# Kernel optimization log

Measured on AMD Instinct MI355X. Metric: run time of the kernel, lower is better.

Reference implementation:

```python
import jax, jax.numpy as jnp
import numpy as np

B, I, R, A, V = 256, 512, 512, 196, 10000

def _linear_params(key, out_dim, in_dim):
    k1, k2 = jax.random.split(key)
    s = 1.0 / np.sqrt(in_dim)
    W = jax.random.uniform(k1, (out_dim, in_dim), minval=-s, maxval=s, dtype=jnp.float32)
    b = jax.random.uniform(k2, (out_dim,), minval=-s, maxval=s, dtype=jnp.float32)
    return W, b

def setup_inputs() -> dict:
    key = jax.random.key(0)
    ks = jax.random.split(key, 16)
    d = {}
    d['x'] = jax.random.normal(ks[0], (B, I), dtype=jnp.float32)
    d['att'] = jax.random.normal(ks[1], (B, A, R), dtype=jnp.float32)
    d['prev_c'] = jax.random.normal(ks[2], (B, R), dtype=jnp.float32)
    d['prev_h'] = jax.random.normal(ks[3], (B, R), dtype=jnp.float32)
    for i, (name, o, inn) in enumerate([('a2a', A, R), ('h2a', A, R), ('d2d', 1, A),
                                         ('i2h', 4 * R, I), ('a2h', 4 * R, R), ('h2h', 4 * R, R),
                                         ('a2a1', A, R), ('h2a1', A, R), ('d2d1', 1, A),
                                         ('proj', V, R)]):
        W, b = _linear_params(ks[4 + i], o, inn)
        d['W_' + name] = W
        d['b_' + name] = b
    return d

def _lin(x, W, b):
    return x @ W.T + b

def _attend(att, h, Wa, ba, Wh, bh, Wd, bd):
    # att: (B, A, R); h: (B, R)
    av = jnp.einsum('bar,or->bao', att, Wa) + ba        # (B, A, A)
    ah = _lin(h, Wh, bh)                                # (B, A)
    dot = jnp.tanh(av + ah[:, :, None])                 # (B, A, A)
    scores = jnp.einsum('bao,o->ba', dot, Wd[0]) + bd[0]  # (B, A)
    w = jax.nn.softmax(scores, axis=-1)
    return jnp.einsum('bar,ba->br', att, w)             # (B, R)

def reference(x, att, prev_c, prev_h,
              W_a2a, b_a2a, W_h2a, b_h2a, W_d2d, b_d2d,
              W_i2h, b_i2h, W_a2h, b_a2h, W_h2h, b_h2h,
              W_a2a1, b_a2a1, W_h2a1, b_h2a1, W_d2d1, b_d2d1,
              W_proj, b_proj):
    # first attention uses prev_h
    prev_att_res = _attend(att, prev_h, W_a2a, b_a2a, W_h2a, b_h2a, W_d2d, b_d2d)
    sums = _lin(x, W_i2h, b_i2h) + _lin(prev_h, W_h2h, b_h2h) + _lin(prev_att_res, W_a2h, b_a2h)
    sig = jax.nn.sigmoid(sums[:, :3 * R])
    in_gate = sig[:, 0:R]
    forget_gate = sig[:, R:2 * R]
    out_gate = sig[:, 2 * R:3 * R]
    in_transform = jnp.tanh(sums[:, 3 * R:4 * R])
    next_c = forget_gate * prev_c + in_gate * in_transform
    next_h = out_gate * jnp.tanh(next_c)
    # second attention uses next_h
    att_res = _attend(att, next_h, W_a2a1, b_a2a1, W_h2a1, b_h2a1, W_d2d1, b_d2d1)
    top_h = att_res + next_h
    logsoft = jax.nn.log_softmax(_lin(top_h, W_proj, b_proj), axis=-1)
    return next_c, top_h, logsoft
```

## Files before the change

kernel.cpp:

```cpp
#include <hip/hip_runtime.h>
#include <math.h>

constexpr int cB  = 256;
constexpr int cI  = 512;
constexpr int cR  = 512;
constexpr int cA  = 196;
constexpr int cV  = 10000;
constexpr int cH4 = 2048;

typedef short bf16x8 __attribute__((ext_vector_type(8)));
typedef float f32x4  __attribute__((ext_vector_type(4)));
typedef unsigned short us8 __attribute__((ext_vector_type(8)));

__device__ inline unsigned short f2bf(float f) {
    unsigned int u = __float_as_uint(f);
    u += 0x7fffu + ((u >> 16) & 1u);
    return (unsigned short)(u >> 16);
}
__device__ inline float bf2f(unsigned short s) {
    return __uint_as_float(((unsigned int)s) << 16);
}
__device__ inline float tanh_f(float x) {
    return 1.f - 2.f / (1.f + __expf(2.f * x));
}

__global__ __launch_bounds__(256) void k_cvt_ah(
    const float* __restrict__ s0, unsigned short* __restrict__ d0, int nb0,
    const float* __restrict__ s1, unsigned short* __restrict__ d1, int nb1,
    const float* __restrict__ s2, unsigned short* __restrict__ d2, int nb2,
    const float* __restrict__ s3, unsigned short* __restrict__ d3, int nb3,
    const float* __restrict__ h, const float* __restrict__ W,
    const float* __restrict__ bias, float* __restrict__ outah)
{
    __shared__ __align__(16) float h_s[cR];
    int blk = blockIdx.x;
    int ncvt = nb0 + nb1 + nb2 + nb3;
    int t = threadIdx.x;
    if (blk < ncvt) {
        const float* src; unsigned short* dst; int base;
        if (blk < nb0)                  { src = s0; dst = d0; base = blk; }
        else if (blk < nb0 + nb1)       { src = s1; dst = d1; base = blk - nb0; }
        else if (blk < nb0 + nb1 + nb2) { src = s2; dst = d2; base = blk - nb0 - nb1; }
        else                            { src = s3; dst = d3; base = blk - nb0 - nb1 - nb2; }
        int i = base * 256 + t;
        float4 v = ((const float4*)src)[i];
        ushort4 b;
        b.x = f2bf(v.x); b.y = f2bf(v.y); b.z = f2bf(v.z); b.w = f2bf(v.w);
        ((ushort4*)dst)[i] = b;
    } else {
        int b = blk - ncvt;
        h_s[t]       = h[b * cR + t];
        h_s[t + 256] = h[b * cR + t + 256];
        __syncthreads();
        if (t < cA) {
            const float4* Wv = (const float4*)(W + (size_t)t * cR);
            const float4* hv = (const float4*)h_s;
            float acc = 0.f;
            #pragma unroll 4
            for (int k = 0; k < cR / 4; ++k) {
                float4 w4 = Wv[k], x4 = hv[k];
                acc += w4.x * x4.x + w4.y * x4.y + w4.z * x4.z + w4.w * x4.w;
            }
            outah[b * cA + t] = acc + bias[t];
        }
    }
}

__global__ __launch_bounds__(256) void k_ah(
    const float* __restrict__ h, const float* __restrict__ W,
    const float* __restrict__ bias, float* __restrict__ out)
{
    __shared__ __align__(16) float h_s[cR];
    int b = blockIdx.x;
    int t = threadIdx.x;
    h_s[t]       = h[b * cR + t];
    h_s[t + 256] = h[b * cR + t + 256];
    __syncthreads();
    if (t < cA) {
        const float4* Wv = (const float4*)(W + (size_t)t * cR);
        const float4* hv = (const float4*)h_s;
        float acc = 0.f;
        #pragma unroll 4
        for (int k = 0; k < cR / 4; ++k) {
            float4 w4 = Wv[k], x4 = hv[k];
            acc += w4.x * x4.x + w4.y * x4.y + w4.z * x4.z + w4.w * x4.w;
        }
        out[b * cA + t] = acc + bias[t];
    }
}

constexpr int SC_LDA = 72;

__global__ __launch_bounds__(256, 2) void k_scores_cv(
    const float* __restrict__ att, unsigned short* __restrict__ att_bf,
    const unsigned short* __restrict__ wa_bf,
    const float* __restrict__ ba, const float* __restrict__ Wd,
    const float* __restrict__ bd, const float* __restrict__ ah,
    float* __restrict__ scores, int wb)
{
    __shared__ __align__(16) unsigned short att_s[128][SC_LDA];
    __shared__ __align__(16) unsigned short wa_s[224][SC_LDA];
    __shared__ float ba_s[224];
    __shared__ float wd_s[224];
    __shared__ float part_s[128][2];

    int tid  = threadIdx.x;
    int wave = tid >> 6;
    int lane = tid & 63;
    int lx   = lane & 15;
    int quad = lane >> 4;
    int mg   = wave >> 1;
    int ng   = wave & 1;
    size_t row0 = (size_t)blockIdx.x * 128;

    if (tid < 224) {
        ba_s[tid] = (tid < cA) ? ba[tid] : 0.f;
        wd_s[tid] = (tid < cA) ? Wd[tid] : 0.f;
    }

    int a_r = tid >> 4, a_c = (tid & 15) * 4;
    int w_r = tid >> 3, w_c = (tid & 7) * 8;
    const float* attA = att + (row0 + a_r) * cR + a_c;
    unsigned short* wbA = att_bf + (row0 + a_r) * cR + a_c;

    f32x4 acc[4][7];
    #pragma unroll
    for (int m = 0; m < 4; ++m)
        #pragma unroll
        for (int c = 0; c < 7; ++c) acc[m][c] = (f32x4){0.f, 0.f, 0.f, 0.f};

    float4 patt[8];
    us8    pwa[7];
    #pragma unroll
    for (int i = 0; i < 8; ++i)
        patt[i] = *(const float4*)(attA + (size_t)i * 16 * cR);
    #pragma unroll
    for (int i = 0; i < 7; ++i) {
        int r = w_r + 32 * i;
        pwa[i] = (r < cA) ? *(const us8*)(wa_bf + (size_t)r * cR + w_c)
                          : (us8){0,0,0,0,0,0,0,0};
    }

    for (int k0 = 0; k0 < cR; k0 += 64) {
        #pragma unroll
        for (int i = 0; i < 8; ++i) {
            float4 v = patt[i];
            ushort4 bv;
            bv.x = f2bf(v.x); bv.y = f2bf(v.y); bv.z = f2bf(v.z); bv.w = f2bf(v.w);
            *(ushort4*)&att_s[a_r + 16 * i][a_c] = bv;
            if (wb)
                *(ushort4*)(wbA + (size_t)i * 16 * cR + k0) = bv;
        }
        #pragma unroll
        for (int i = 0; i < 7; ++i)
            *(us8*)&wa_s[w_r + 32 * i][w_c] = pwa[i];
        if (k0 + 64 < cR) {
            #pragma unroll
            for (int i = 0; i < 8; ++i)
                patt[i] = *(const float4*)(attA + (size_t)i * 16 * cR + k0 + 64);
            #pragma unroll
            for (int i = 0; i < 7; ++i) {
                int r = w_r + 32 * i;
                pwa[i] = (r < cA) ? *(const us8*)(wa_bf + (size_t)r * cR + k0 + 64 + w_c)
                                  : (us8){0,0,0,0,0,0,0,0};
            }
        }
        __syncthreads();
        #pragma unroll
        for (int ks = 0; ks < 2; ++ks) {
            int kb = ks * 32 + quad * 8;
            bf16x8 af[4];
            #pragma unroll
            for (int m = 0; m < 4; ++m)
                af[m] = *(const bf16x8*)&att_s[mg * 64 + m * 16 + lx][kb];
            #pragma unroll
            for (int c = 0; c < 7; ++c) {
                bf16x8 bfr = *(const bf16x8*)&wa_s[ng * 112 + c * 16 + lx][kb];
                #pragma unroll
                for (int m = 0; m < 4; ++m)
                    acc[m][c] = __builtin_amdgcn_mfma_f32_16x16x32_bf16(af[m], bfr, acc[m][c], 0, 0, 0);
            }
        }
        __syncthreads();
    }

    #pragma unroll
    for (int m = 0; m < 4; ++m) {
        #pragma unroll
        for (int reg = 0; reg < 4; ++reg) {
            int rl = mg * 64 + m * 16 + quad * 4 + reg;
            float ahv = ah[row0 + rl];
            float part = 0.f;
            #pragma unroll
            for (int c = 0; c < 7; ++c) {
                int col = ng * 112 + c * 16 + lx;
                part += tanh_f(acc[m][c][reg] + ba_s[col] + ahv) * wd_s[col];
            }
            part += __shfl_xor(part, 1);
            part += __shfl_xor(part, 2);
            part += __shfl_xor(part, 4);
            part += __shfl_xor(part, 8);
            if (lx == 0) part_s[rl][ng] = part;
        }
    }
    __syncthreads();
    if (tid < 128)
        scores[row0 + tid] = part_s[tid][0] + part_s[tid][1] + bd[0];
}

__global__ __launch_bounds__(256, 2) void k_scores_bf(
    const unsigned short* __restrict__ att_bf,
    const unsigned short* __restrict__ wa_bf,
    const float* __restrict__ ba, const float* __restrict__ Wd,
    const float* __restrict__ bd, const float* __restrict__ ah,
    float* __restrict__ scores)
{
    __shared__ __align__(16) unsigned short att_s[128][SC_LDA];
    __shared__ __align__(16) unsigned short wa_s[224][SC_LDA];
    __shared__ float ba_s[224];
    __shared__ float wd_s[224];
    __shared__ float part_s[128][2];

    int tid  = threadIdx.x;
    int wave = tid >> 6;
    int lane = tid & 63;
    int lx   = lane & 15;
    int quad = lane >> 4;
    int mg   = wave >> 1;
    int ng   = wave & 1;
    size_t row0 = (size_t)blockIdx.x * 128;

    if (tid < 224) {
        ba_s[tid] = (tid < cA) ? ba[tid] : 0.f;
        wd_s[tid] = (tid < cA) ? Wd[tid] : 0.f;
    }

    int a_r = tid >> 3, a_c = (tid & 7) * 8;
    int w_r = tid >> 3, w_c = (tid & 7) * 8;
    const unsigned short* attA = att_bf + (row0 + a_r) * cR + a_c;

    f32x4 acc[4][7];
    #pragma unroll
    for (int m = 0; m < 4; ++m)
        #pragma unroll
        for (int c = 0; c < 7; ++c) acc[m][c] = (f32x4){0.f, 0.f, 0.f, 0.f};

    us8 patt[4];
    us8 pwa[7];
    #pragma unroll
    for (int i = 0; i < 4; ++i)
        patt[i] = *(const us8*)(attA + (size_t)i * 32 * cR);
    #pragma unroll
    for (int i = 0; i < 7; ++i) {
        int r = w_r + 32 * i;
        pwa[i] = (r < cA) ? *(const us8*)(wa_bf + (size_t)r * cR + w_c)
                          : (us8){0,0,0,0,0,0,0,0};
    }

    for (int k0 = 0; k0 < cR; k0 += 64) {
        #pragma unroll
        for (int i = 0; i < 4; ++i)
            *(us8*)&att_s[a_r + 32 * i][a_c] = patt[i];
        #pragma unroll
        for (int i = 0; i < 7; ++i)
            *(us8*)&wa_s[w_r + 32 * i][w_c] = pwa[i];
        if (k0 + 64 < cR) {
            #pragma unroll
            for (int i = 0; i < 4; ++i)
                patt[i] = *(const us8*)(attA + (size_t)i * 32 * cR + k0 + 64);
            #pragma unroll
            for (int i = 0; i < 7; ++i) {
                int r = w_r + 32 * i;
                pwa[i] = (r < cA) ? *(const us8*)(wa_bf + (size_t)r * cR + k0 + 64 + w_c)
                                  : (us8){0,0,0,0,0,0,0,0};
            }
        }
        __syncthreads();
        #pragma unroll
        for (int ks = 0; ks < 2; ++ks) {
            int kb = ks * 32 + quad * 8;
            bf16x8 af[4];
            #pragma unroll
            for (int m = 0; m < 4; ++m)
                af[m] = *(const bf16x8*)&att_s[mg * 64 + m * 16 + lx][kb];
            #pragma unroll
            for (int c = 0; c < 7; ++c) {
                bf16x8 bfr = *(const bf16x8*)&wa_s[ng * 112 + c * 16 + lx][kb];
                #pragma unroll
                for (int m = 0; m < 4; ++m)
                    acc[m][c] = __builtin_amdgcn_mfma_f32_16x16x32_bf16(af[m], bfr, acc[m][c], 0, 0, 0);
            }
        }
        __syncthreads();
    }

    #pragma unroll
    for (int m = 0; m < 4; ++m) {
        #pragma unroll
        for (int reg = 0; reg < 4; ++reg) {
            int rl = mg * 64 + m * 16 + quad * 4 + reg;
            float ahv = ah[row0 + rl];
            float part = 0.f;
            #pragma unroll
            for (int c = 0; c < 7; ++c) {
                int col = ng * 112 + c * 16 + lx;
                part += tanh_f(acc[m][c][reg] + ba_s[col] + ahv) * wd_s[col];
            }
            part += __shfl_xor(part, 1);
            part += __shfl_xor(part, 2);
            part += __shfl_xor(part, 4);
            part += __shfl_xor(part, 8);
            if (lx == 0) part_s[rl][ng] = part;
        }
    }
    __syncthreads();
    if (tid < 128)
        scores[row0 + tid] = part_s[tid][0] + part_s[tid][1] + bd[0];
}

__device__ inline void softmax_w(const float* scores, int b, int t, float* red,
                                 float* w_s)
{
    float s = (t < cA) ? scores[b * cA + t] : -INFINITY;
    red[t] = s; __syncthreads();
    for (int off = 128; off > 0; off >>= 1) {
        if (t < off) red[t] = fmaxf(red[t], red[t + off]);
        __syncthreads();
    }
    float mx = red[0];
    __syncthreads();
    float e = (t < cA) ? __expf(s - mx) : 0.f;
    red[t] = e; __syncthreads();
    for (int off = 128; off > 0; off >>= 1) {
        if (t < off) red[t] += red[t + off];
        __syncthreads();
    }
    float inv = 1.f / red[0];
    if (t < cA) w_s[t] = e * inv;
    __syncthreads();
}

__global__ __launch_bounds__(256) void k_attres_bf(
    const float* __restrict__ scores, const unsigned short* __restrict__ att_bf,
    const float* __restrict__ addin,
    float* __restrict__ out, unsigned short* __restrict__ out_bf)
{
    __shared__ float red[256];
    __shared__ float w_s[cA];
    __shared__ float red2[4][512];
    int b = blockIdx.x, t = threadIdx.x;
    softmax_w(scores, b, t, red, w_s);

    int p = t >> 6, l = t & 63;
    const unsigned short* base = att_bf + (size_t)b * cA * cR + l * 8;
    float acc[8] = {};
    #pragma unroll 7
    for (int a = p; a < cA; a += 4) {
        us8 v = *(const us8*)(base + (size_t)a * cR);
        float w = w_s[a];
        #pragma unroll
        for (int j = 0; j < 8; ++j)
            acc[j] += bf2f(v[j]) * w;
    }
    #pragma unroll
    for (int j = 0; j < 8; ++j)
        red2[p][l * 8 + j] = acc[j];
    __syncthreads();
    #pragma unroll
    for (int rr = 0; rr < 2; ++rr) {
        int r = t + rr * 256;
        float s = red2[0][r] + red2[1][r] + red2[2][r] + red2[3][r];
        if (addin) s += addin[b * cR + r];
        out[b * cR + r] = s;
        out_bf[b * cR + r] = f2bf(s);
    }
}

__global__ __launch_bounds__(256) void k_attres_f32(
    const float* __restrict__ scores, const float* __restrict__ att,
    const float* __restrict__ addin,
    float* __restrict__ out, unsigned short* __restrict__ out_bf)
{
    __shared__ float red[256];
    __shared__ float w_s[cA];
    int b = blockIdx.x, t = threadIdx.x;
    softmax_w(scores, b, t, red, w_s);

    const float* attb = att + (size_t)b * cA * cR + 2 * t;
    float acc0 = 0.f, acc1 = 0.f;
    #pragma unroll 4
    for (int a = 0; a < cA; ++a) {
        float2 u = *(const float2*)(attb + (size_t)a * cR);
        float w = w_s[a];
        acc0 += u.x * w;
        acc1 += u.y * w;
    }
    if (addin) {
        acc0 += addin[b * cR + 2 * t];
        acc1 += addin[b * cR + 2 * t + 1];
    }
    out[b * cR + 2 * t]     = acc0;
    out[b * cR + 2 * t + 1] = acc1;
    out_bf[b * cR + 2 * t]     = f2bf(acc0);
    out_bf[b * cR + 2 * t + 1] = f2bf(acc1);
}

__global__ __launch_bounds__(256, 4) void k_sums(
    const unsigned short* __restrict__ x_bf,
    const unsigned short* __restrict__ h_bf,
    const unsigned short* __restrict__ ar_bf,
    const float* __restrict__ Wi, const float* __restrict__ Wh,
    const float* __restrict__ Wa,
    const float* __restrict__ bi, const float* __restrict__ bh,
    const float* __restrict__ ba, float* __restrict__ out)
{
    __shared__ __align__(16) unsigned short a_s[32][SC_LDA];
    __shared__ __align__(16) unsigned short w_s[64][SC_LDA];
    int tid  = threadIdx.x;
    int wave = tid >> 6;
    int lane = tid & 63;
    int lx   = lane & 15;
    int quad = lane >> 4;
    int b0 = blockIdx.x * 32;
    int j0 = blockIdx.y * 64;

    const unsigned short* Aarr[3] = {x_bf, h_bf, ar_bf};
    const float* Warr[3] = {Wi, Wh, Wa};

    int a_r = tid >> 3, a_c = (tid & 7) * 8;
    int w_r = tid >> 4, w_c = (tid & 15) * 4;

    f32x4 acc0 = {0.f, 0.f, 0.f, 0.f}, acc1 = {0.f, 0.f, 0.f, 0.f};

    us8 pa;
    float4 pw[4];
    pa = *(const us8*)(Aarr[0] + (size_t)(b0 + a_r) * cR + a_c);
    #pragma unroll
    for (int i = 0; i < 4; ++i)
        pw[i] = *(const float4*)(Warr[0] + (size_t)(j0 + w_r + 16 * i) * cR + w_c);

    for (int it = 0; it < 24; ++it) {
        *(us8*)&a_s[a_r][a_c] = pa;
        #pragma unroll
        for (int i = 0; i < 4; ++i) {
            float4 v = pw[i];
            ushort4 bv;
            bv.x = f2bf(v.x); bv.y = f2bf(v.y); bv.z = f2bf(v.z); bv.w = f2bf(v.w);
            *(ushort4*)&w_s[w_r + 16 * i][w_c] = bv;
        }
        if (it < 23) {
            int s2 = (it + 1) >> 3, k2 = ((it + 1) & 7) * 64;
            pa = *(const us8*)(Aarr[s2] + (size_t)(b0 + a_r) * cR + k2 + a_c);
            #pragma unroll
            for (int i = 0; i < 4; ++i)
                pw[i] = *(const float4*)(Warr[s2] + (size_t)(j0 + w_r + 16 * i) * cR + k2 + w_c);
        }
        __syncthreads();
        #pragma unroll
        for (int ks = 0; ks < 2; ++ks) {
            int kb = ks * 32 + quad * 8;
            bf16x8 afr0 = *(const bf16x8*)&a_s[lx][kb];
            bf16x8 afr1 = *(const bf16x8*)&a_s[16 + lx][kb];
            bf16x8 bfr  = *(const bf16x8*)&w_s[wave * 16 + lx][kb];
            acc0 = __builtin_amdgcn_mfma_f32_16x16x32_bf16(afr0, bfr, acc0, 0, 0, 0);
            acc1 = __builtin_amdgcn_mfma_f32_16x16x32_bf16(afr1, bfr, acc1, 0, 0, 0);
        }
        __syncthreads();
    }
    int j = j0 + wave * 16 + lx;
    float bsum = bi[j] + bh[j] + ba[j];
    #pragma unroll
    for (int reg = 0; reg < 4; ++reg) {
        int b = b0 + quad * 4 + reg;
        out[(size_t)b * cH4 + j]        = acc0[reg] + bsum;
        out[(size_t)(b + 16) * cH4 + j] = acc1[reg] + bsum;
    }
}

__global__ __launch_bounds__(256, 3) void k_lin(
    const unsigned short* __restrict__ in_bf, const float* __restrict__ W,
    const float* __restrict__ bias, float* __restrict__ out, int N)
{
    __shared__ __align__(16) unsigned short a_s[128][SC_LDA];
    __shared__ __align__(16) unsigned short w_s[64][SC_LDA];
    int tid  = threadIdx.x;
    int wave = tid >> 6;
    int lane = tid & 63;
    int lx   = lane & 15;
    int quad = lane >> 4;
    int mg   = wave >> 1;
    int ng   = wave & 1;
    int b0 = blockIdx.x * 128;
    int j0 = blockIdx.y * 64;

    int a_r = tid >> 3, a_c = (tid & 7) * 8;
    int w_r = tid >> 4, w_c = (tid & 15) * 4;

    f32x4 acc[4][2];
    #pragma unroll
    for (int m = 0; m < 4; ++m)
        #pragma unroll
        for (int c = 0; c < 2; ++c) acc[m][c] = (f32x4){0.f, 0.f, 0.f, 0.f};

    us8 pa[4];
    float4 pw[4];
    #pragma unroll
    for (int i = 0; i < 4; ++i)
        pa[i] = *(const us8*)(in_bf + (size_t)(b0 + a_r + 32 * i) * cR + a_c);
    #pragma unroll
    for (int i = 0; i < 4; ++i) {
        int r = j0 + w_r + 16 * i;
        pw[i] = (r < N) ? *(const float4*)(W + (size_t)r * cR + w_c)
                        : make_float4(0.f, 0.f, 0.f, 0.f);
    }

    for (int k0 = 0; k0 < cR; k0 += 64) {
        #pragma unroll
        for (int i = 0; i < 4; ++i)
            *(us8*)&a_s[a_r + 32 * i][a_c] = pa[i];
        #pragma unroll
        for (int i = 0; i < 4; ++i) {
            float4 v = pw[i];
            ushort4 bv;
            bv.x = f2bf(v.x); bv.y = f2bf(v.y); bv.z = f2bf(v.z); bv.w = f2bf(v.w);
            *(ushort4*)&w_s[w_r + 16 * i][w_c] = bv;
        }
        if (k0 + 64 < cR) {
            #pragma unroll
            for (int i = 0; i < 4; ++i)
                pa[i] = *(const us8*)(in_bf + (size_t)(b0 + a_r + 32 * i) * cR + k0 + 64 + a_c);
            #pragma unroll
            for (int i = 0; i < 4; ++i) {
                int r = j0 + w_r + 16 * i;
                pw[i] = (r < N) ? *(const float4*)(W + (size_t)r * cR + k0 + 64 + w_c)
                                : make_float4(0.f, 0.f, 0.f, 0.f);
            }
        }
        __syncthreads();
        #pragma unroll
        for (int ks = 0; ks < 2; ++ks) {
            int kb = ks * 32 + quad * 8;
            bf16x8 af[4];
            #pragma unroll
            for (int m = 0; m < 4; ++m)
                af[m] = *(const bf16x8*)&a_s[mg * 64 + m * 16 + lx][kb];
            #pragma unroll
            for (int c = 0; c < 2; ++c) {
                bf16x8 bfr = *(const bf16x8*)&w_s[ng * 32 + c * 16 + lx][kb];
                #pragma unroll
                for (int m = 0; m < 4; ++m)
                    acc[m][c] = __builtin_amdgcn_mfma_f32_16x16x32_bf16(af[m], bfr, acc[m][c], 0, 0, 0);
            }
        }
        __syncthreads();
    }
    #pragma unroll
    for (int c = 0; c < 2; ++c) {
        int j = j0 + ng * 32 + c * 16 + lx;
        if (j < N) {
            float bv = bias[j];
            #pragma unroll
            for (int m = 0; m < 4; ++m) {
                #pragma unroll
                for (int reg = 0; reg < 4; ++reg) {
                    int b = b0 + mg * 64 + m * 16 + quad * 4 + reg;
                    out[(size_t)b * N + j] = acc[m][c][reg] + bv;
                }
            }
        }
    }
}

__global__ __launch_bounds__(256) void k_cell(
    const float* __restrict__ sums, const float* __restrict__ prev_c,
    float* __restrict__ next_c, float* __restrict__ next_h)
{
    int idx = blockIdx.x * 256 + threadIdx.x;
    int b = idx >> 9;
    int j = idx & 511;
    const float* srow = sums + (size_t)b * cH4;
    float ig = 1.f / (1.f + __expf(-srow[j]));
    float fg = 1.f / (1.f + __expf(-srow[cR + j]));
    float og = 1.f / (1.f + __expf(-srow[2 * cR + j]));
    float gt = tanh_f(srow[3 * cR + j]);
    float c = fg * prev_c[idx] + ig * gt;
    float hh = og * tanh_f(c);
    next_c[idx] = c;
    next_h[idx] = hh;
}

__global__ __launch_bounds__(256) void k_logsoftmax(float* __restrict__ logits)
{
    __shared__ float red[256];
    int b = blockIdx.x, t = threadIdx.x;
    float* row = logits + (size_t)b * cV;
    const float4* row4 = (const float4*)row;
    float mx = -INFINITY;
    for (int v = t; v < cV / 4; v += 256) {
        float4 f = row4[v];
        mx = fmaxf(mx, fmaxf(fmaxf(f.x, f.y), fmaxf(f.z, f.w)));
    }
    red[t] = mx; __syncthreads();
    for (int off = 128; off > 0; off >>= 1) {
        if (t < off) red[t] = fmaxf(red[t], red[t + off]);
        __syncthreads();
    }
    mx = red[0]; __syncthreads();
    float sum = 0.f;
    for (int v = t; v < cV / 4; v += 256) {
        float4 f = row4[v];
        sum += __expf(f.x - mx) + __expf(f.y - mx) + __expf(f.z - mx) + __expf(f.w - mx);
    }
    red[t] = sum; __syncthreads();
    for (int off = 128; off > 0; off >>= 1) {
        if (t < off) red[t] += red[t + off];
        __syncthreads();
    }
    float lse = mx + logf(red[0]);
    for (int v = t; v < cV / 4; v += 256) {
        float4 f = row4[v];
        f.x -= lse; f.y -= lse; f.z -= lse; f.w -= lse;
        ((float4*)row)[v] = f;
    }
}

extern "C" void kernel_launch(void* const* d_in, const int* in_sizes, int n_in,
                              void* d_out, int out_size, void* d_ws, size_t ws_size,
                              hipStream_t stream)
{
    const float* x      = (const float*)d_in[0];
    const float* att    = (const float*)d_in[1];
    const float* prev_c = (const float*)d_in[2];
    const float* prev_h = (const float*)d_in[3];
    const float* W_a2a  = (const float*)d_in[4];
    const float* b_a2a  = (const float*)d_in[5];
    const float* W_h2a  = (const float*)d_in[6];
    const float* b_h2a  = (const float*)d_in[7];
    const float* W_d2d  = (const float*)d_in[8];
    const float* b_d2d  = (const float*)d_in[9];
    const float* W_i2h  = (const float*)d_in[10];
    const float* b_i2h  = (const float*)d_in[11];
    const float* W_a2h  = (const float*)d_in[12];
    const float* b_a2h  = (const float*)d_in[13];
    const float* W_h2h  = (const float*)d_in[14];
    const float* b_h2h  = (const float*)d_in[15];
    const float* W_a2a1 = (const float*)d_in[16];
    const float* b_a2a1 = (const float*)d_in[17];
    const float* W_h2a1 = (const float*)d_in[18];
    const float* b_h2a1 = (const float*)d_in[19];
    const float* W_d2d1 = (const float*)d_in[20];
    const float* b_d2d1 = (const float*)d_in[21];
    const float* W_proj = (const float*)d_in[22];
    const float* b_proj = (const float*)d_in[23];

    float* out_next_c = (float*)d_out;
    float* out_top_h  = out_next_c + (size_t)cB * cR;
    float* out_logits = out_top_h  + (size_t)cB * cR;

    const size_t ATT_FLOATS = 12845056;
    const size_t NEED_A = (ATT_FLOATS + 1445888) * sizeof(float);
    bool bigws = ws_size >= NEED_A;

    float* ws = (float*)d_ws;
    unsigned short* att_bf = (unsigned short*)ws;
    float* p = bigws ? (ws + ATT_FLOATS) : ws;
    unsigned short* wa2a_bf  = (unsigned short*)p;  p += 50176;
    unsigned short* wa2a1_bf = (unsigned short*)p;  p += 50176;
    unsigned short* x_bf     = (unsigned short*)p;  p += 65536;
    unsigned short* h_bf     = (unsigned short*)p;  p += 65536;
    unsigned short* ar1_bf   = (unsigned short*)p;  p += 65536;
    unsigned short* ar2_bf   = (unsigned short*)p;  p += 65536;
    unsigned short* toph_bf  = (unsigned short*)p;  p += 65536;
    float* ws_ah      = p;  p += 50176;
    float* ws_scores  = p;  p += 50176;
    float* ws_attres1 = p;  p += 131072;
    float* ws_attres2 = p;  p += 131072;
    float* ws_sums    = p;  p += 524288;
    float* ws_next_h  = p;  p += 131072;

    k_cvt_ah<<<452 + cB, 256, 0, stream>>>(W_a2a, wa2a_bf, 98,
                                           W_a2a1, wa2a1_bf, 98,
                                           x, x_bf, 128,
                                           prev_h, h_bf, 128,
                                           prev_h, W_h2a, b_h2a, ws_ah);

    k_scores_cv<<<(cB * cA) / 128, 256, 0, stream>>>(att, att_bf, wa2a_bf,
                                                     b_a2a, W_d2d, b_d2d,
                                                     ws_ah, ws_scores,
                                                     bigws ? 1 : 0);
    if (bigws)
        k_attres_bf<<<cB, 256, 0, stream>>>(ws_scores, att_bf, nullptr,
                                            ws_attres1, ar1_bf);
    else
        k_attres_f32<<<cB, 256, 0, stream>>>(ws_scores, att, nullptr,
                                             ws_attres1, ar1_bf);

    k_sums<<<dim3(8, 32), 256, 0, stream>>>(x_bf, h_bf, ar1_bf,
                                            W_i2h, W_h2h, W_a2h,
                                            b_i2h, b_h2h, b_a2h, ws_sums);
    k_cell<<<(cB * cR) / 256, 256, 0, stream>>>(ws_sums, prev_c, out_next_c, ws_next_h);

    k_ah<<<cB, 256, 0, stream>>>(ws_next_h, W_h2a1, b_h2a1, ws_ah);
    if (bigws) {
        k_scores_bf<<<(cB * cA) / 128, 256, 0, stream>>>(att_bf, wa2a1_bf,
                                                         b_a2a1, W_d2d1, b_d2d1,
                                                         ws_ah, ws_scores);
        k_attres_bf<<<cB, 256, 0, stream>>>(ws_scores, att_bf, ws_next_h,
                                            out_top_h, toph_bf);
    } else {
        k_scores_cv<<<(cB * cA) / 128, 256, 0, stream>>>(att, att_bf, wa2a1_bf,
                                                         b_a2a1, W_d2d1, b_d2d1,
                                                         ws_ah, ws_scores, 0);
        k_attres_f32<<<cB, 256, 0, stream>>>(ws_scores, att, ws_next_h,
                                             out_top_h, toph_bf);
    }

    k_lin<<<dim3(2, 157), 256, 0, stream>>>(toph_bf, W_proj, b_proj, out_logits, cV);
    k_logsoftmax<<<cB, 256, 0, stream>>>(out_logits);
}
```

Measured before the change: 362.4 us.

## Compute both attention projections in one MFMA pass and fuse cell with h2a

A new scores kernel multiplies each att tile against both W_a2a and W_a2a1 in one pass. It finishes the first attention's scores and stores the second attention's pre-activation projection (bf16) to workspace, so the second large GEMM becomes a light tanh-dot kernel once next_h is known. The LSTM cell is fused with the h2a linear, attres uses 512 threads, and logsoftmax uses a single-pass online max/sum. This needs about 20 MB of extra workspace and falls back to the old path when the workspace is too small.

```diff
diff --git a/kernel.cpp b/kernel.cpp
--- a/kernel.cpp
+++ b/kernel.cpp
@@ -7,6 +7,7 @@
 constexpr int cA  = 196;
 constexpr int cV  = 10000;
 constexpr int cH4 = 2048;
+constexpr int AV2_LD = 200;
 
 typedef short bf16x8 __attribute__((ext_vector_type(8)));
 typedef float f32x4  __attribute__((ext_vector_type(4)));
@@ -91,6 +92,181 @@
 
 constexpr int SC_LDA = 72;
 
+__global__ __launch_bounds__(512, 2) void k_scores2g(
+    const float* __restrict__ att, unsigned short* __restrict__ att_bf,
+    const unsigned short* __restrict__ wa1_bf,
+    const unsigned short* __restrict__ wa2_bf,
+    const float* __restrict__ ba1, const float* __restrict__ ba2,
+    const float* __restrict__ Wd1, const float* __restrict__ bd1,
+    const float* __restrict__ ah, float* __restrict__ scores,
+    unsigned short* __restrict__ av2)
+{
+    __shared__ __align__(16) unsigned short att_s[128][SC_LDA];
+    __shared__ __align__(16) unsigned short wa_s[448][SC_LDA];
+    __shared__ float ba1_s[224];
+    __shared__ float ba2_s[224];
+    __shared__ float wd_s[224];
+    __shared__ float part_s[128][2];
+
+    int tid  = threadIdx.x;
+    int wave = tid >> 6;
+    int lane = tid & 63;
+    int lx   = lane & 15;
+    int quad = lane >> 4;
+    int mg   = wave >> 2;
+    int ng   = wave & 3;
+    size_t row0 = (size_t)blockIdx.x * 128;
+
+    if (tid < 224) {
+        ba1_s[tid] = (tid < cA) ? ba1[tid] : 0.f;
+        ba2_s[tid] = (tid < cA) ? ba2[tid] : 0.f;
+        wd_s[tid]  = (tid < cA) ? Wd1[tid] : 0.f;
+    }
+
+    int a_r = tid >> 4, a_c = (tid & 15) * 4;
+    int w_r = tid >> 3, w_c = (tid & 7) * 8;
+    const float* attA = att + (row0 + a_r) * cR + a_c;
+    unsigned short* wbA = att_bf + (row0 + a_r) * cR + a_c;
+
+    f32x4 acc[4][7];
+    #pragma unroll
+    for (int m = 0; m < 4; ++m)
+        #pragma unroll
+        for (int c = 0; c < 7; ++c) acc[m][c] = (f32x4){0.f, 0.f, 0.f, 0.f};
+
+    float4 patt[4];
+    us8    pwa[7];
+    #pragma unroll
+    for (int i = 0; i < 4; ++i)
+        patt[i] = *(const float4*)(attA + (size_t)i * 32 * cR);
+    #pragma unroll
+    for (int i = 0; i < 7; ++i) {
+        int R = w_r + 64 * i;
+        const unsigned short* src = (R < 224) ? wa1_bf : wa2_bf;
+        int rr = (R < 224) ? R : R - 224;
+        pwa[i] = (rr < cA) ? *(const us8*)(src + (size_t)rr * cR + w_c)
+                           : (us8){0,0,0,0,0,0,0,0};
+    }
+
+    for (int k0 = 0; k0 < cR; k0 += 64) {
+        #pragma unroll
+        for (int i = 0; i < 4; ++i) {
+            float4 v = patt[i];
+            ushort4 bv;
+            bv.x = f2bf(v.x); bv.y = f2bf(v.y); bv.z = f2bf(v.z); bv.w = f2bf(v.w);
+            *(ushort4*)&att_s[a_r + 32 * i][a_c] = bv;
+            *(ushort4*)(wbA + (size_t)i * 32 * cR + k0) = bv;
+        }
+        #pragma unroll
+        for (int i = 0; i < 7; ++i)
+            *(us8*)&wa_s[w_r + 64 * i][w_c] = pwa[i];
+        if (k0 + 64 < cR) {
+            #pragma unroll
+            for (int i = 0; i < 4; ++i)
+                patt[i] = *(const float4*)(attA + (size_t)i * 32 * cR + k0 + 64);
+            #pragma unroll
+            for (int i = 0; i < 7; ++i) {
+                int R = w_r + 64 * i;
+                const unsigned short* src = (R < 224) ? wa1_bf : wa2_bf;
+                int rr = (R < 224) ? R : R - 224;
+                pwa[i] = (rr < cA) ? *(const us8*)(src + (size_t)rr * cR + k0 + 64 + w_c)
+                                   : (us8){0,0,0,0,0,0,0,0};
+            }
+        }
+        __syncthreads();
+        #pragma unroll
+        for (int ks = 0; ks < 2; ++ks) {
+            int kb = ks * 32 + quad * 8;
+            bf16x8 af[4];
+            #pragma unroll
+            for (int m = 0; m < 4; ++m)
+                af[m] = *(const bf16x8*)&att_s[mg * 64 + m * 16 + lx][kb];
+            #pragma unroll
+            for (int c = 0; c < 7; ++c) {
+                bf16x8 bfr = *(const bf16x8*)&wa_s[ng * 112 + c * 16 + lx][kb];
+                #pragma unroll
+                for (int m = 0; m < 4; ++m)
+                    acc[m][c] = __builtin_amdgcn_mfma_f32_16x16x32_bf16(af[m], bfr, acc[m][c], 0, 0, 0);
+            }
+        }
+        __syncthreads();
+    }
+
+    if (ng < 2) {
+        #pragma unroll
+        for (int m = 0; m < 4; ++m) {
+            #pragma unroll
+            for (int reg = 0; reg < 4; ++reg) {
+                int rl = mg * 64 + m * 16 + quad * 4 + reg;
+                float ahv = ah[row0 + rl];
+                float part = 0.f;
+                #pragma unroll
+                for (int c = 0; c < 7; ++c) {
+                    int col = ng * 112 + c * 16 + lx;
+                    part += tanh_f(acc[m][c][reg] + ba1_s[col] + ahv) * wd_s[col];
+                }
+                part += __shfl_xor(part, 1);
+                part += __shfl_xor(part, 2);
+                part += __shfl_xor(part, 4);
+                part += __shfl_xor(part, 8);
+                if (lx == 0) part_s[rl][ng] = part;
+            }
+        }
+    } else {
+        int cb = (ng - 2) * 112;
+        #pragma unroll
+        for (int m = 0; m < 4; ++m) {
+            #pragma unroll
+            for (int reg = 0; reg < 4; ++reg) {
+                int rl = mg * 64 + m * 16 + quad * 4 + reg;
+                size_t ro = (size_t)(row0 + rl) * AV2_LD;
+                #pragma unroll
+                for (int c = 0; c < 7; ++c) {
+                    int col = cb + c * 16 + lx;
+                    float v = acc[m][c][reg] + ba2_s[col];
+                    if (col < cA)          av2[ro + col] = f2bf(v);
+                    else if (col < AV2_LD) av2[ro + col] = 0;
+                }
+            }
+        }
+    }
+    __syncthreads();
+    if (tid < 128)
+        scores[row0 + tid] = part_s[tid][0] + part_s[tid][1] + bd1[0];
+}
+
+__global__ __launch_bounds__(256) void k_dot2(
+    const unsigned short* __restrict__ av2, const float* __restrict__ ah,
+    const float* __restrict__ Wd, const float* __restrict__ bd,
+    float* __restrict__ scores)
+{
+    __shared__ float wd_s[AV2_LD];
+    int t = threadIdx.x;
+    if (t < AV2_LD) wd_s[t] = (t < cA) ? Wd[t] : 0.f;
+    __syncthreads();
+    int wave = t >> 6, half = (t >> 5) & 1, L = t & 31;
+    int r = blockIdx.x * 8 + wave * 2 + half;
+    int b = r / cA;
+    float s = 0.f;
+    if (L < 25) {
+        us8 v = *(const us8*)(av2 + (size_t)r * AV2_LD + L * 8);
+        const float* ap = ah + (size_t)b * cA + L * 8;
+        float4 a0 = *(const float4*)(ap);
+        float4 a1 = (L < 24) ? *(const float4*)(ap + 4)
+                             : make_float4(0.f, 0.f, 0.f, 0.f);
+        float av[8] = {a0.x, a0.y, a0.z, a0.w, a1.x, a1.y, a1.z, a1.w};
+        #pragma unroll
+        for (int j = 0; j < 8; ++j)
+            s += tanh_f(bf2f(v[j]) + av[j]) * wd_s[L * 8 + j];
+    }
+    s += __shfl_xor(s, 1);
+    s += __shfl_xor(s, 2);
+    s += __shfl_xor(s, 4);
+    s += __shfl_xor(s, 8);
+    s += __shfl_xor(s, 16);
+    if (L == 0) scores[r] = s + bd[0];
+}
+
 __global__ __launch_bounds__(256, 2) void k_scores_cv(
     const float* __restrict__ att, unsigned short* __restrict__ att_bf,
     const unsigned short* __restrict__ wa_bf,
@@ -340,22 +516,39 @@
     __syncthreads();
 }
 
-__global__ __launch_bounds__(256) void k_attres_bf(
+__global__ __launch_bounds__(512) void k_attres_bf(
     const float* __restrict__ scores, const unsigned short* __restrict__ att_bf,
     const float* __restrict__ addin,
     float* __restrict__ out, unsigned short* __restrict__ out_bf)
 {
-    __shared__ float red[256];
+    __shared__ float red[512];
     __shared__ float w_s[cA];
-    __shared__ float red2[4][512];
+    __shared__ float red2[8][512];
     int b = blockIdx.x, t = threadIdx.x;
-    softmax_w(scores, b, t, red, w_s);
+
+    float s = (t < cA) ? scores[b * cA + t] : -INFINITY;
+    red[t] = s; __syncthreads();
+    for (int off = 256; off > 0; off >>= 1) {
+        if (t < off) red[t] = fmaxf(red[t], red[t + off]);
+        __syncthreads();
+    }
+    float mx = red[0];
+    __syncthreads();
+    float e = (t < cA) ? __expf(s - mx) : 0.f;
+    red[t] = e; __syncthreads();
+    for (int off = 256; off > 0; off >>= 1) {
+        if (t < off) red[t] += red[t + off];
+        __syncthreads();
+    }
+    float inv = 1.f / red[0];
+    if (t < cA) w_s[t] = e * inv;
+    __syncthreads();
 
     int p = t >> 6, l = t & 63;
     const unsigned short* base = att_bf + (size_t)b * cA * cR + l * 8;
     float acc[8] = {};
-    #pragma unroll 7
-    for (int a = p; a < cA; a += 4) {
+    #pragma unroll 4
+    for (int a = p; a < cA; a += 8) {
         us8 v = *(const us8*)(base + (size_t)a * cR);
         float w = w_s[a];
         #pragma unroll
@@ -366,13 +559,13 @@
     for (int j = 0; j < 8; ++j)
         red2[p][l * 8 + j] = acc[j];
     __syncthreads();
-    #pragma unroll
-    for (int rr = 0; rr < 2; ++rr) {
-        int r = t + rr * 256;
-        float s = red2[0][r] + red2[1][r] + red2[2][r] + red2[3][r];
-        if (addin) s += addin[b * cR + r];
-        out[b * cR + r] = s;
-        out_bf[b * cR + r] = f2bf(s);
+    {
+        int r = t;
+        float s2 = red2[0][r] + red2[1][r] + red2[2][r] + red2[3][r]
+                 + red2[4][r] + red2[5][r] + red2[6][r] + red2[7][r];
+        if (addin) s2 += addin[b * cR + r];
+        out[b * cR + r] = s2;
+        out_bf[b * cR + r] = f2bf(s2);
     }
 }
 
@@ -568,6 +761,42 @@
                 }
             }
         }
+    }
+}
+
+__global__ __launch_bounds__(256) void k_cell_ah(
+    const float* __restrict__ sums, const float* __restrict__ prev_c,
+    const float* __restrict__ W, const float* __restrict__ bias,
+    float* __restrict__ next_c, float* __restrict__ next_h,
+    float* __restrict__ outah)
+{
+    __shared__ __align__(16) float h_s[cR];
+    int b = blockIdx.x, t = threadIdx.x;
+    const float* srow = sums + (size_t)b * cH4;
+    #pragma unroll
+    for (int rr = 0; rr < 2; ++rr) {
+        int j = t + rr * 256;
+        float ig = 1.f / (1.f + __expf(-srow[j]));
+        float fg = 1.f / (1.f + __expf(-srow[cR + j]));
+        float og = 1.f / (1.f + __expf(-srow[2 * cR + j]));
+        float gt = tanh_f(srow[3 * cR + j]);
+        float c = fg * prev_c[b * cR + j] + ig * gt;
+        float h = og * tanh_f(c);
+        next_c[b * cR + j] = c;
+        next_h[b * cR + j] = h;
+        h_s[j] = h;
+    }
+    __syncthreads();
+    if (t < cA) {
+        const float4* Wv = (const float4*)(W + (size_t)t * cR);
+        const float4* hv = (const float4*)h_s;
+        float acc = 0.f;
+        #pragma unroll 4
+        for (int k = 0; k < cR / 4; ++k) {
+            float4 w4 = Wv[k], x4 = hv[k];
+            acc += w4.x * x4.x + w4.y * x4.y + w4.z * x4.z + w4.w * x4.w;
+        }
+        outah[b * cA + t] = acc + bias[t];
     }
 }
 
@@ -591,32 +820,31 @@
 
 __global__ __launch_bounds__(256) void k_logsoftmax(float* __restrict__ logits)
 {
-    __shared__ float red[256];
+    __shared__ float red_m[256];
+    __shared__ float red_d[256];
     int b = blockIdx.x, t = threadIdx.x;
     float* row = logits + (size_t)b * cV;
     const float4* row4 = (const float4*)row;
-    float mx = -INFINITY;
+    float m = -INFINITY, d = 0.f;
     for (int v = t; v < cV / 4; v += 256) {
         float4 f = row4[v];
-        mx = fmaxf(mx, fmaxf(fmaxf(f.x, f.y), fmaxf(f.z, f.w)));
-    }
-    red[t] = mx; __syncthreads();
+        float m4 = fmaxf(fmaxf(f.x, f.y), fmaxf(f.z, f.w));
+        float nm = fmaxf(m, m4);
+        d = d * __expf(m - nm) + __expf(f.x - nm) + __expf(f.y - nm)
+          + __expf(f.z - nm) + __expf(f.w - nm);
+        m = nm;
+    }
+    red_m[t] = m; red_d[t] = d; __syncthreads();
     for (int off = 128; off > 0; off >>= 1) {
-        if (t < off) red[t] = fmaxf(red[t], red[t + off]);
-        __syncthreads();
-    }
-    mx = red[0]; __syncthreads();
-    float sum = 0.f;
-    for (int v = t; v < cV / 4; v += 256) {
-        float4 f = row4[v];
-        sum += __expf(f.x - mx) + __expf(f.y - mx) + __expf(f.z - mx) + __expf(f.w - mx);
-    }
-    red[t] = sum; __syncthreads();
-    for (int off = 128; off > 0; off >>= 1) {
-        if (t < off) red[t] += red[t + off];
-        __syncthreads();
-    }
-    float lse = mx + logf(red[0]);
+        if (t < off) {
+            float m2 = red_m[t + off], d2 = red_d[t + off];
+            float M = fmaxf(red_m[t], m2);
+            red_d[t] = red_d[t] * __expf(red_m[t] - M) + d2 * __expf(m2 - M);
+            red_m[t] = M;
+        }
+        __syncthreads();
+    }
+    float lse = red_m[0] + logf(red_d[0]);
     for (int v = t; v < cV / 4; v += 256) {
         float4 f = row4[v];
         f.x -= lse; f.y -= lse; f.z -= lse; f.w -= lse;
@@ -658,12 +886,15 @@
     float* out_logits = out_top_h  + (size_t)cB * cR;
 
     const size_t ATT_FLOATS = 12845056;
+    const size_t AV2_FLOATS = 5017600;
     const size_t NEED_A = (ATT_FLOATS + 1445888) * sizeof(float);
-    bool bigws = ws_size >= NEED_A;
+    const size_t NEED_B = (ATT_FLOATS + 1445888 + AV2_FLOATS) * sizeof(float);
+    bool bigA = ws_size >= NEED_A;
+    bool bigB = ws_size >= NEED_B;
 
     float* ws = (float*)d_ws;
     unsigned short* att_bf = (unsigned short*)ws;
-    float* p = bigws ? (ws + ATT_FLOATS) : ws;
+    float* p = bigA ? (ws + ATT_FLOATS) : ws;
     unsigned short* wa2a_bf  = (unsigned short*)p;  p += 50176;
     unsigned short* wa2a1_bf = (unsigned short*)p;  p += 50176;
     unsigned short* x_bf     = (unsigned short*)p;  p += 65536;
@@ -677,6 +908,7 @@
     float* ws_attres2 = p;  p += 131072;
     float* ws_sums    = p;  p += 524288;
     float* ws_next_h  = p;  p += 131072;
+    unsigned short* av2 = (unsigned short*)p;
 
     k_cvt_ah<<<452 + cB, 256, 0, stream>>>(W_a2a, wa2a_bf, 98,
                                            W_a2a1, wa2a1_bf, 98,
@@ -684,30 +916,49 @@
                                            prev_h, h_bf, 128,
                                            prev_h, W_h2a, b_h2a, ws_ah);
 
-    k_scores_cv<<<(cB * cA) / 128, 256, 0, stream>>>(att, att_bf, wa2a_bf,
-                                                     b_a2a, W_d2d, b_d2d,
-                                                     ws_ah, ws_scores,
-                                                     bigws ? 1 : 0);
-    if (bigws)
-        k_attres_bf<<<cB, 256, 0, stream>>>(ws_scores, att_bf, nullptr,
+    if (bigB) {
+        k_scores2g<<<(cB * cA) / 128, 512, 0, stream>>>(
+            att, att_bf, wa2a_bf, wa2a1_bf, b_a2a, b_a2a1,
+            W_d2d, b_d2d, ws_ah, ws_scores, av2);
+        k_attres_bf<<<cB, 512, 0, stream>>>(ws_scores, att_bf, nullptr,
                                             ws_attres1, ar1_bf);
-    else
-        k_attres_f32<<<cB, 256, 0, stream>>>(ws_scores, att, nullptr,
-                                             ws_attres1, ar1_bf);
-
-    k_sums<<<dim3(8, 32), 256, 0, stream>>>(x_bf, h_bf, ar1_bf,
-                                            W_i2h, W_h2h, W_a2h,
-                                            b_i2h, b_h2h, b_a2h, ws_sums);
-    k_cell<<<(cB * cR) / 256, 256, 0, stream>>>(ws_sums, prev_c, out_next_c, ws_next_h);
-
-    k_ah<<<cB, 256, 0, stream>>>(ws_next_h, W_h2a1, b_h2a1, ws_ah);
-    if (bigws) {
+        k_sums<<<dim3(8, 32), 256, 0, stream>>>(x_bf, h_bf, ar1_bf,
+                                                W_i2h, W_h2h, W_a2h,
+                                                b_i2h, b_h2h, b_a2h, ws_sums);
+        k_cell_ah<<<cB, 256, 0, stream>>>(ws_sums, prev_c, W_h2a1, b_h2a1,
+                                          out_next_c, ws_next_h, ws_ah);
+        k_dot2<<<(cB * cA) / 8, 256, 0, stream>>>(av2, ws_ah, W_d2d1, b_d2d1,
+                                                  ws_scores);
+        k_attres_bf<<<cB, 512, 0, stream>>>(ws_scores, att_bf, ws_next_h,
+                                            out_top_h, toph_bf);
+    } else if (bigA) {
+        k_scores_cv<<<(cB * cA) / 128, 256, 0, stream>>>(att, att_bf, wa2a_bf,
+                                                         b_a2a, W_d2d, b_d2d,
+                                                         ws_ah, ws_scores, 1);
+        k_attres_bf<<<cB, 512, 0, stream>>>(ws_scores, att_bf, nullptr,
+                                            ws_attres1, ar1_bf);
+        k_sums<<<dim3(8, 32), 256, 0, stream>>>(x_bf, h_bf, ar1_bf,
+                                                W_i2h, W_h2h, W_a2h,
+                                                b_i2h, b_h2h, b_a2h, ws_sums);
+        k_cell_ah<<<cB, 256, 0, stream>>>(ws_sums, prev_c, W_h2a1, b_h2a1,
+                                          out_next_c, ws_next_h, ws_ah);
         k_scores_bf<<<(cB * cA) / 128, 256, 0, stream>>>(att_bf, wa2a1_bf,
                                                          b_a2a1, W_d2d1, b_d2d1,
                                                          ws_ah, ws_scores);
-        k_attres_bf<<<cB, 256, 0, stream>>>(ws_scores, att_bf, ws_next_h,
+        k_attres_bf<<<cB, 512, 0, stream>>>(ws_scores, att_bf, ws_next_h,
                                             out_top_h, toph_bf);
     } else {
+        k_scores_cv<<<(cB * cA) / 128, 256, 0, stream>>>(att, att_bf, wa2a_bf,
+                                                         b_a2a, W_d2d, b_d2d,
+                                                         ws_ah, ws_scores, 0);
+        k_attres_f32<<<cB, 256, 0, stream>>>(ws_scores, att, nullptr,
+                                             ws_attres1, ar1_bf);
+        k_sums<<<dim3(8, 32), 256, 0, stream>>>(x_bf, h_bf, ar1_bf,
+                                                W_i2h, W_h2h, W_a2h,
+                                                b_i2h, b_h2h, b_a2h, ws_sums);
+        k_cell<<<(cB * cR) / 256, 256, 0, stream>>>(ws_sums, prev_c,
+                                                    out_next_c, ws_next_h);
+        k_ah<<<cB, 256, 0, stream>>>(ws_next_h, W_h2a1, b_h2a1, ws_ah);
         k_scores_cv<<<(cB * cA) / 128, 256, 0, stream>>>(att, att_bf, wa2a1_bf,
                                                          b_a2a1, W_d2d1, b_d2d1,
                                                          ws_ah, ws_scores, 0);
```

After: 356.9 us. About the same (-1.5%).
